# Performance work log

Hardware: AMD Instinct MI355X
Metric: run time of the kernel (lower is better)

Reference implementation:

```python
import jax, jax.numpy as jnp
import numpy as np

B, N, DIM = 4, 1024, 1024
HEADS, DH = 16, 64
INNER = HEADS * DH          # 1024
PROJ_H = max(16, DH // 8)   # 16
TOP_K = 256
TEMP = 1.0
SCALE = DH ** -0.5
LN_EPS = 1e-5


def setup_inputs() -> dict:
    key = jax.random.key(0)
    ks = jax.random.split(key, 9)
    s = 0.02
    return {
        "x": jax.random.normal(ks[0], (B, N, DIM), dtype=jnp.float32),
        "w_qkv": jax.random.normal(ks[1], (3 * INNER, DIM), dtype=jnp.float32) * s,
        "w_out": jax.random.normal(ks[2], (DIM, INNER), dtype=jnp.float32) * s,
        "b_out": jnp.zeros((DIM,), dtype=jnp.float32),
        "ln_g": jnp.ones((DH,), dtype=jnp.float32),
        "ln_b": jnp.zeros((DH,), dtype=jnp.float32),
        "w1": jax.random.normal(ks[3], (PROJ_H, DH), dtype=jnp.float32) * s,
        "b1": jnp.zeros((PROJ_H,), dtype=jnp.float32),
        "w2": jax.random.normal(ks[4], (1, PROJ_H), dtype=jnp.float32) * s,
        "b2": jnp.zeros((1,), dtype=jnp.float32),
    }


def _soma_gate(token_feat, ln_g, ln_b, w1, b1, w2, b2):
    # token_feat: [B, N, DH] -> gate [B, N] in (0,1)
    mu = token_feat.mean(axis=-1, keepdims=True)
    var = token_feat.var(axis=-1, keepdims=True)
    H = (token_feat - mu) * jax.lax.rsqrt(var + LN_EPS) * ln_g + ln_b
    h = jax.nn.gelu(H @ w1.T + b1, approximate=False)
    scores = (h @ w2.T + b2)[..., 0]                       # [B, N]
    scores = scores / (TEMP + 1e-12)
    # top-k soft mask: non-topk positions set to -1e9 before sigmoid
    topk_vals, topk_idx = jax.lax.top_k(scores, TOP_K)
    b_idx = jnp.arange(scores.shape[0])[:, None]
    scores = jnp.full_like(scores, -1e9).at[b_idx, topk_idx].set(topk_vals)
    return jax.nn.sigmoid(scores)


def reference(x, w_qkv, w_out, b_out, ln_g, ln_b, w1, b1, w2, b2):
    Bx, Nx, _ = x.shape
    qkv = x @ w_qkv.T                                      # [B, N, 3*INNER]
    q, k, v = jnp.split(qkv, 3, axis=-1)
    to_heads = lambda t: t.reshape(Bx, Nx, HEADS, DH).transpose(0, 2, 1, 3)
    q, k, v = to_heads(q), to_heads(k), to_heads(v)        # [B, H, N, DH]

    dots = jnp.einsum('bhid,bhjd->bhij', q, k) * SCALE     # [B, H, N, N]

    q_mean = q.mean(axis=1)                                # [B, N, DH]
    gate = _soma_gate(q_mean, ln_g, ln_b, w1, b1, w2, b2)  # [B, N]
    dots = dots * (gate[:, None, :, None] * gate[:, None, None, :])

    attn = jax.nn.softmax(dots, axis=-1)
    out = jnp.einsum('bhij,bhjd->bhid', attn, v)           # [B, H, N, DH]
    out = out.transpose(0, 2, 1, 3).reshape(Bx, Nx, INNER)
    return out @ w_out.T + b_out
```

## Files before the change

kernel.cpp:

```cpp
#include <hip/hip_runtime.h>
#include <hip/hip_bf16.h>
#include <stdint.h>

typedef __bf16 bf16;
typedef __bf16 bf16x8 __attribute__((ext_vector_type(8)));
typedef float floatx4 __attribute__((ext_vector_type(4)));

typedef const __attribute__((address_space(1))) uint32_t glb_u32;
typedef __attribute__((address_space(3))) uint32_t lds_u32;

__device__ __forceinline__ void cp16(void* lds, const void* gp) {
    __builtin_amdgcn_global_load_lds((glb_u32*)gp, (lds_u32*)lds, 16, 0, 0);
}

#define MFMA16(a, b, c) __builtin_amdgcn_mfma_f32_16x16x32_bf16((a), (b), (c), 0, 0, 0)
#define SCALE_ 0.125f

__global__ __launch_bounds__(256) void k_cvt_prep(
    const float* __restrict__ x, const float* __restrict__ wq,
    const float* __restrict__ wo, bf16* __restrict__ xb,
    bf16* __restrict__ xl, bf16* __restrict__ wqb, bf16* __restrict__ wob,
    bf16* __restrict__ whl) {
    if (blockIdx.x < 4096) {
        size_t i8 = ((size_t)blockIdx.x * 256 + threadIdx.x) * 8;
        const float* src; bf16* dst; size_t off; bool isx = false;
        if (i8 < 4194304)      { src = x;  dst = xb;  off = i8; isx = true; }
        else if (i8 < 7340032) { src = wq; dst = wqb; off = i8 - 4194304; }
        else                   { src = wo; dst = wob; off = i8 - 7340032; }
        float4 a = *(const float4*)(src + off);
        float4 b = *(const float4*)(src + off + 4);
        union { bf16 h[8]; uint4 u; } hi, lo;
        hi.h[0] = (bf16)a.x; hi.h[1] = (bf16)a.y; hi.h[2] = (bf16)a.z; hi.h[3] = (bf16)a.w;
        hi.h[4] = (bf16)b.x; hi.h[5] = (bf16)b.y; hi.h[6] = (bf16)b.z; hi.h[7] = (bf16)b.w;
        *(uint4*)(dst + off) = hi.u;
        if (isx) {
            lo.h[0] = (bf16)(a.x - (float)hi.h[0]);
            lo.h[1] = (bf16)(a.y - (float)hi.h[1]);
            lo.h[2] = (bf16)(a.z - (float)hi.h[2]);
            lo.h[3] = (bf16)(a.w - (float)hi.h[3]);
            lo.h[4] = (bf16)(b.x - (float)hi.h[4]);
            lo.h[5] = (bf16)(b.y - (float)hi.h[5]);
            lo.h[6] = (bf16)(b.z - (float)hi.h[6]);
            lo.h[7] = (bf16)(b.w - (float)hi.h[7]);
            *(uint4*)(xl + off) = lo.u;
        }
    } else {
        int t = (blockIdx.x - 4096) * 256 + threadIdx.x;
        int k = t & 1023, d = t >> 10;
        float s = 0.f;
        #pragma unroll
        for (int h = 0; h < 16; ++h) s += wq[(size_t)(h * 64 + d) * 1024 + k];
        s *= (1.f / 16.f);
        bf16 hi = (bf16)s;
        whl[(size_t)d * 1024 + k] = hi;
        whl[(size_t)(64 + d) * 1024 + k] = (bf16)(s - (float)hi);
    }
}

__global__ __launch_bounds__(256) void k_score_gemm(
    const bf16* __restrict__ xh, const bf16* __restrict__ xl,
    const bf16* __restrict__ whl, float* __restrict__ qmbuf) {
    __shared__ bf16 Ah[128 * 32];
    __shared__ bf16 Al[128 * 32];
    __shared__ bf16 Bs[128 * 32];
    const int t = threadIdx.x;
    const int lane = t & 63;
    const int w = t >> 6;
    const int m0 = blockIdx.x * 128;
    const int srow = t >> 2;
    const int scol = (t & 3) * 8;
    const int fr = lane & 15;
    const int kc = (lane >> 4) * 8;
    const int wm0 = w * 32;

    floatx4 zero4 = {0.f, 0.f, 0.f, 0.f};
    floatx4 acc[2][4];
    #pragma unroll
    for (int i = 0; i < 2; ++i)
        #pragma unroll
        for (int j = 0; j < 4; ++j) acc[i][j] = zero4;

    for (int k0 = 0; k0 < 1024; k0 += 32) {
        __syncthreads();
        cp16(Ah + t * 8,        xh + (size_t)(m0 + srow) * 1024 + k0 + scol);
        cp16(Ah + t * 8 + 2048, xh + (size_t)(m0 + srow + 64) * 1024 + k0 + scol);
        cp16(Al + t * 8,        xl + (size_t)(m0 + srow) * 1024 + k0 + scol);
        cp16(Al + t * 8 + 2048, xl + (size_t)(m0 + srow + 64) * 1024 + k0 + scol);
        cp16(Bs + t * 8,        whl + (size_t)srow * 1024 + k0 + scol);
        cp16(Bs + t * 8 + 2048, whl + (size_t)(srow + 64) * 1024 + k0 + scol);
        __syncthreads();
        bf16x8 ah[2], al[2], bh[4], bl[4];
        #pragma unroll
        for (int mi = 0; mi < 2; ++mi) {
            ah[mi] = *(const bf16x8*)&Ah[(wm0 + mi * 16 + fr) * 32 + kc];
            al[mi] = *(const bf16x8*)&Al[(wm0 + mi * 16 + fr) * 32 + kc];
        }
        #pragma unroll
        for (int ni = 0; ni < 4; ++ni) {
            bh[ni] = *(const bf16x8*)&Bs[(ni * 16 + fr) * 32 + kc];
            bl[ni] = *(const bf16x8*)&Bs[(64 + ni * 16 + fr) * 32 + kc];
        }
        #pragma unroll
        for (int mi = 0; mi < 2; ++mi)
            #pragma unroll
            for (int ni = 0; ni < 4; ++ni) {
                acc[mi][ni] = MFMA16(ah[mi], bh[ni], acc[mi][ni]);
                acc[mi][ni] = MFMA16(ah[mi], bl[ni], acc[mi][ni]);
                acc[mi][ni] = MFMA16(al[mi], bh[ni], acc[mi][ni]);
            }
    }

    const int rowb = (lane >> 4) * 4;
    #pragma unroll
    for (int mi = 0; mi < 2; ++mi)
        #pragma unroll
        for (int ni = 0; ni < 4; ++ni)
            #pragma unroll
            for (int r = 0; r < 4; ++r) {
                const int row = m0 + wm0 + mi * 16 + rowb + r;
                qmbuf[(size_t)row * 64 + ni * 16 + fr] = acc[mi][ni][r];
            }
}

__global__ __launch_bounds__(256) void k_score_tail(
    const float* __restrict__ qmbuf, const float* __restrict__ lng,
    const float* __restrict__ lnb, const float* __restrict__ w1f,
    const float* __restrict__ b1f, const float* __restrict__ w2f,
    const float* __restrict__ b2f, float* __restrict__ scores) {
    const int w = threadIdx.x >> 6, lane = threadIdx.x & 63;
    const int r = blockIdx.x * 4 + w;
    __shared__ float Hs[4][64];
    __shared__ float hh[4][16];

    float qm = qmbuf[(size_t)r * 64 + lane];
    float s = qm;
    #pragma unroll
    for (int off = 32; off > 0; off >>= 1) s += __shfl_xor(s, off);
    float mu = s * (1.f / 64.f);
    float dx = qm - mu;
    float v2 = dx * dx;
    #pragma unroll
    for (int off = 32; off > 0; off >>= 1) v2 += __shfl_xor(v2, off);
    float var = v2 * (1.f / 64.f);
    float H = dx * (1.0f / sqrtf(var + 1e-5f)) * lng[lane] + lnb[lane];
    Hs[w][lane] = H;
    if (lane < 16) {
        float a = b1f[lane];
        #pragma unroll
        for (int d = 0; d < 64; ++d) a += Hs[w][d] * w1f[lane * 64 + d];
        hh[w][lane] = 0.5f * a * (1.0f + erff(a * 0.70710678118654752f));
    }
    if (lane == 0) {
        float sc = b2f[0];
        #pragma unroll
        for (int p = 0; p < 16; ++p) sc += hh[w][p] * w2f[p];
        scores[r] = sc;
    }
}

__global__ __launch_bounds__(256) void k_topk(const float* __restrict__ scores,
                                              float* __restrict__ gate,
                                              int* __restrict__ idx,
                                              float* __restrict__ gsel) {
    const int w = threadIdx.x >> 6, lane = threadIdx.x & 63;
    const float* sc = scores + w * 1024;
    float s[16];
    uint32_t key[16];
    #pragma unroll
    for (int i = 0; i < 16; ++i) {
        s[i] = sc[lane * 16 + i];
        uint32_t u = __float_as_uint(s[i]);
        key[i] = (u >> 31) ? ~u : (u | 0x80000000u);
    }
    uint32_t prefix = 0;
    for (int bit = 31; bit >= 0; --bit) {
        uint32_t cand = prefix | (1u << bit);
        int c = 0;
        #pragma unroll
        for (int i = 0; i < 16; ++i) c += (key[i] >= cand);
        #pragma unroll
        for (int off = 1; off < 64; off <<= 1) c += __shfl_xor(c, off);
        if (c >= 256) prefix = cand;
    }
    int cg = 0, eq = 0;
    #pragma unroll
    for (int i = 0; i < 16; ++i) { cg += (key[i] > prefix); eq += (key[i] == prefix); }
    #pragma unroll
    for (int off = 1; off < 64; off <<= 1) cg += __shfl_xor(cg, off);
    const int quota = 256 - cg;
    int xs = eq;
    #pragma unroll
    for (int off = 1; off < 64; off <<= 1) {
        int y = __shfl_up(xs, off);
        if (lane >= off) xs += y;
    }
    int run = xs - eq;
    bool selv[16];
    int cnt = 0;
    #pragma unroll
    for (int i = 0; i < 16; ++i) {
        bool sel = key[i] > prefix;
        if (key[i] == prefix) { sel = (run < quota); run++; }
        selv[i] = sel;
        cnt += sel ? 1 : 0;
        gate[w * 1024 + lane * 16 + i] = sel ? 1.0f / (1.0f + expf(-s[i])) : 0.0f;
    }
    int xc = cnt;
    #pragma unroll
    for (int off = 1; off < 64; off <<= 1) {
        int y = __shfl_up(xc, off);
        if (lane >= off) xc += y;
    }
    int pos = xc - cnt;
    #pragma unroll
    for (int i = 0; i < 16; ++i) {
        if (selv[i]) {
            idx[w * 256 + pos]  = lane * 16 + i;
            gsel[w * 256 + pos] = 1.0f / (1.0f + expf(-s[i]));
            pos++;
        }
    }
}

__global__ __launch_bounds__(256) void k_qkv_sel(
    const bf16* __restrict__ xb, const bf16* __restrict__ wqb,
    const int* __restrict__ idx, bf16* __restrict__ qsel,
    bf16* __restrict__ ksel, bf16* __restrict__ vbuf) {
    __shared__ bf16 As[128 * 32];
    __shared__ bf16 Bs[128 * 32];
    const int t = threadIdx.x;
    const int lane = t & 63;
    const int w = t >> 6;
    const int srow = t >> 2;
    const int scol = (t & 3) * 8;
    const int wm = (w & 1) * 64;
    const int wn = (w >> 1) * 64;
    const int fr = lane & 15;
    const int kc = (lane >> 4) * 8;

    const int bid = blockIdx.x;
    const bool isV = bid < 256;
    int n0, m0;
    size_t abase1, abase2;
    const bf16* Bsrc;
    if (isV) {
        n0 = (bid & 7) * 128;
        m0 = (bid >> 3) * 128;
        Bsrc = wqb + (size_t)(2048 + n0) * 1024;
        abase1 = (size_t)(m0 + srow) * 1024;
        abase2 = (size_t)(m0 + srow + 64) * 1024;
    } else {
        int q = bid - 256;
        n0 = (q & 15) * 128;
        m0 = (q >> 4) * 128;
        Bsrc = wqb + (size_t)n0 * 1024;
        const int mg1 = m0 + srow, mg2 = mg1 + 64;
        const int tok1 = idx[(mg1 >> 8) * 256 + (mg1 & 255)];
        const int tok2 = idx[(mg2 >> 8) * 256 + (mg2 & 255)];
        abase1 = ((size_t)(mg1 >> 8) * 1024 + tok1) * 1024;
        abase2 = ((size_t)(mg2 >> 8) * 1024 + tok2) * 1024;
    }

    floatx4 zero4 = {0.f, 0.f, 0.f, 0.f};
    floatx4 acc[4][4];
    #pragma unroll
    for (int i = 0; i < 4; ++i)
        #pragma unroll
        for (int j = 0; j < 4; ++j) acc[i][j] = zero4;

    for (int k0 = 0; k0 < 1024; k0 += 32) {
        __syncthreads();
        cp16(As + t * 8,        xb + abase1 + k0 + scol);
        cp16(As + t * 8 + 2048, xb + abase2 + k0 + scol);
        cp16(Bs + t * 8,        Bsrc + (size_t)srow * 1024 + k0 + scol);
        cp16(Bs + t * 8 + 2048, Bsrc + (size_t)(srow + 64) * 1024 + k0 + scol);
        __syncthreads();
        bf16x8 a[4], b[4];
        #pragma unroll
        for (int mi = 0; mi < 4; ++mi)
            a[mi] = *(const bf16x8*)&As[(wm + mi * 16 + fr) * 32 + kc];
        #pragma unroll
        for (int ni = 0; ni < 4; ++ni)
            b[ni] = *(const bf16x8*)&Bs[(wn + ni * 16 + fr) * 32 + kc];
        #pragma unroll
        for (int mi = 0; mi < 4; ++mi)
            #pragma unroll
            for (int ni = 0; ni < 4; ++ni)
                acc[mi][ni] = MFMA16(a[mi], b[ni], acc[mi][ni]);
    }

    const int rowb = (lane >> 4) * 4;
    #pragma unroll
    for (int ni = 0; ni < 4; ++ni) {
        const int n_base = n0 + wn + ni * 16;
        if (isV) {
            const int h = n_base >> 6;
            const int dd = (n_base & 63) + fr;
            #pragma unroll
            for (int mi = 0; mi < 4; ++mi)
                #pragma unroll
                for (int r = 0; r < 4; ++r) {
                    const int mg = m0 + wm + mi * 16 + rowb + r;
                    const int bb = mg >> 10, nq = mg & 1023;
                    vbuf[(((size_t)(bb * 16 + h)) * 1024 + nq) * 64 + dd] =
                        (bf16)acc[mi][ni][r];
                }
        } else {
            const int region = n_base >> 10;
            const int nn = n_base & 1023;
            const int h = nn >> 6;
            const int dd = (nn & 63) + fr;
            #pragma unroll
            for (int mi = 0; mi < 4; ++mi)
                #pragma unroll
                for (int r = 0; r < 4; ++r) {
                    const int mg = m0 + wm + mi * 16 + rowb + r;
                    const bf16 v = (bf16)acc[mi][ni][r];
                    if (region == 0) {
                        qsel[(size_t)mg * 1024 + h * 64 + dd] = v;
                    } else {
                        const int b = mg >> 8, s = mg & 255;
                        ksel[(((size_t)(b * 16 + h)) * 256 + s) * 64 + dd] = v;
                    }
                }
        }
    }
}

__global__ __launch_bounds__(256) void k_vgather(
    const bf16* __restrict__ vbuf, const int* __restrict__ idx,
    bf16* __restrict__ VselT, float* __restrict__ SumVuns,
    bf16* __restrict__ qsel) {
    const int bh = blockIdx.x, b = bh >> 4, h = bh & 15;
    const int t = threadIdx.x, w = t >> 6, lane = t & 63;
    const bf16* vb = vbuf + (size_t)bh * 65536;
    bf16* Vo = VselT + (size_t)bh * 16384;

    __shared__ bf16 Vt[64][72];
    __shared__ float redAll[4][64];
    __shared__ float redSel[4][64];

    float sAll = 0.f;
    for (int j = w * 256; j < w * 256 + 256; ++j)
        sAll += (float)vb[(size_t)j * 64 + lane];
    redAll[w][lane] = sAll;

    const int d = t & 63, sg = t >> 6;
    const int s_loc = t >> 2, part = t & 3;
    float sSel = 0.f;

    for (int c = 0; c < 4; ++c) {
        __syncthreads();
        int j = idx[b * 256 + c * 64 + s_loc];
        const uint4* vsrc = (const uint4*)(vb + (size_t)j * 64 + part * 16);
        uint4 v0 = vsrc[0], v1 = vsrc[1];
        *(uint4*)&Vt[s_loc][part * 16]     = v0;
        *(uint4*)&Vt[s_loc][part * 16 + 8] = v1;
        __syncthreads();
        union { bf16 h_[16]; uint4 u[2]; } tmp;
        #pragma unroll
        for (int u = 0; u < 16; ++u) {
            bf16 v = Vt[sg * 16 + u][d];
            tmp.h_[u] = v;
            sSel += (float)v;
        }
        uint4* vdst = (uint4*)(Vo + (size_t)d * 256 + c * 64 + sg * 16);
        vdst[0] = tmp.u[0]; vdst[1] = tmp.u[1];
    }
    redSel[sg][d] = sSel;
    __syncthreads();
    if (t < 64) {
        float sa = redAll[0][t] + redAll[1][t] + redAll[2][t] + redAll[3][t];
        float ss = redSel[0][t] + redSel[1][t] + redSel[2][t] + redSel[3][t];
        SumVuns[bh * 64 + t] = sa - ss;
        qsel[(size_t)(1024 + b) * 1024 + h * 64 + t] = (bf16)(sa * (1.f / 1024.f));
    }
}

__global__ __launch_bounds__(256) void k_attn(
    bf16* __restrict__ qsel, const bf16* __restrict__ Ksel,
    const bf16* __restrict__ VselT, const float* __restrict__ gsel,
    const float* __restrict__ SumVuns) {
    const int bh = blockIdx.x;
    const int qt = blockIdx.y;
    const int b = bh >> 4, h = bh & 15;
    const int t = threadIdx.x, w = t >> 6, lane = t & 63;
    const int m0 = qt * 64;
    const bf16* kb = Ksel + (size_t)bh * 16384;
    const bf16* vb = VselT + (size_t)bh * 16384;

    __shared__ bf16 Qs[64 * 72];
    __shared__ bf16 Ks[64 * 72];
    __shared__ bf16 Vs[64 * 72];
    __shared__ bf16 Ps[4][16 * 72];

    #pragma unroll
    for (int c = 0; c < 2; ++c) {
        int idx2 = t + 256 * c, row = idx2 >> 3, c8 = (idx2 & 7) * 8;
        *(uint4*)&Qs[row * 72 + c8] =
            *(const uint4*)&qsel[(size_t)(b * 256 + m0 + row) * 1024 + h * 64 + c8];
    }
    const int fr = lane & 15;
    const int kq = lane >> 4;
    const int rowb = kq * 4;
    __syncthreads();
    bf16x8 aq[2];
    aq[0] = *(const bf16x8*)&Qs[(w * 16 + fr) * 72 + kq * 8];
    aq[1] = *(const bf16x8*)&Qs[(w * 16 + fr) * 72 + 32 + kq * 8];

    float gq[4];
    #pragma unroll
    for (int r = 0; r < 4; ++r)
        gq[r] = gsel[b * 256 + m0 + w * 16 + rowb + r] * SCALE_;

    float mrow[4] = {0.f, 0.f, 0.f, 0.f};
    float lrow[4] = {0.f, 0.f, 0.f, 0.f};
    floatx4 zero4 = {0.f, 0.f, 0.f, 0.f};
    floatx4 Of[4] = {zero4, zero4, zero4, zero4};

    for (int jt = 0; jt < 4; ++jt) {
        const int j0 = jt * 64;
        __syncthreads();
        #pragma unroll
        for (int c = 0; c < 2; ++c) {
            int idx2 = t + 256 * c, row = idx2 >> 3, c8 = (idx2 & 7) * 8;
            *(uint4*)&Ks[row * 72 + c8] = *(const uint4*)&kb[(size_t)(j0 + row) * 64 + c8];
            *(uint4*)&Vs[row * 72 + c8] = *(const uint4*)&vb[(size_t)row * 256 + j0 + c8];
        }
        __syncthreads();

        floatx4 S[4] = {zero4, zero4, zero4, zero4};
        #pragma unroll
        for (int ks = 0; ks < 2; ++ks) {
            #pragma unroll
            for (int ni = 0; ni < 4; ++ni) {
                bf16x8 bfr = *(const bf16x8*)&Ks[(ni * 16 + fr) * 72 + ks * 32 + kq * 8];
                S[ni] = MFMA16(aq[ks], bfr, S[ni]);
            }
        }
        float gk[4];
        #pragma unroll
        for (int ni = 0; ni < 4; ++ni) gk[ni] = gsel[b * 256 + j0 + ni * 16 + fr];

        float p[4][4], rmax[4] = {0.f, 0.f, 0.f, 0.f};
        #pragma unroll
        for (int ni = 0; ni < 4; ++ni)
            #pragma unroll
            for (int r = 0; r < 4; ++r) {
                float sv = S[ni][r] * (gq[r] * gk[ni]);
                p[ni][r] = sv;
                rmax[r] = fmaxf(rmax[r], sv);
            }
        #pragma unroll
        for (int r = 0; r < 4; ++r) {
            #pragma unroll
            for (int off = 1; off < 16; off <<= 1)
                rmax[r] = fmaxf(rmax[r], __shfl_xor(rmax[r], off));
        }
        float alpha[4], rsum[4] = {0.f, 0.f, 0.f, 0.f};
        #pragma unroll
        for (int r = 0; r < 4; ++r) {
            float mn = fmaxf(mrow[r], rmax[r]);
            alpha[r] = __expf(mrow[r] - mn);
            mrow[r] = mn;
        }
        #pragma unroll
        for (int ni = 0; ni < 4; ++ni)
            #pragma unroll
            for (int r = 0; r < 4; ++r) {
                float pv = __expf(p[ni][r] - mrow[r]);
                p[ni][r] = pv;
                rsum[r] += pv;
            }
        #pragma unroll
        for (int r = 0; r < 4; ++r) {
            #pragma unroll
            for (int off = 1; off < 16; off <<= 1) rsum[r] += __shfl_xor(rsum[r], off);
            lrow[r] = lrow[r] * alpha[r] + rsum[r];
        }
        #pragma unroll
        for (int nd = 0; nd < 4; ++nd)
            #pragma unroll
            for (int r = 0; r < 4; ++r) Of[nd][r] *= alpha[r];

        #pragma unroll
        for (int ni = 0; ni < 4; ++ni)
            #pragma unroll
            for (int r = 0; r < 4; ++r)
                Ps[w][(rowb + r) * 72 + ni * 16 + fr] = (bf16)p[ni][r];

        #pragma unroll
        for (int ks = 0; ks < 2; ++ks) {
            bf16x8 ap = *(const bf16x8*)&Ps[w][fr * 72 + ks * 32 + kq * 8];
            #pragma unroll
            for (int nd = 0; nd < 4; ++nd) {
                bf16x8 bv = *(const bf16x8*)&Vs[(nd * 16 + fr) * 72 + ks * 32 + kq * 8];
                Of[nd] = MFMA16(ap, bv, Of[nd]);
            }
        }
    }

    #pragma unroll
    for (int nd = 0; nd < 4; ++nd)
        #pragma unroll
        for (int r = 0; r < 4; ++r) {
            float em = __expf(-mrow[r]);
            float num = Of[nd][r] + em * SumVuns[bh * 64 + nd * 16 + fr];
            float den = lrow[r] + 768.0f * em;
            qsel[(size_t)(b * 256 + m0 + w * 16 + rowb + r) * 1024 +
                 h * 64 + nd * 16 + fr] = (bf16)(num / den);
        }
}

__global__ __launch_bounds__(256) void k_out_sel(
    const bf16* __restrict__ A, const bf16* __restrict__ wob,
    const float* __restrict__ b_out, const int* __restrict__ idx,
    float* __restrict__ ubase, float* __restrict__ out) {
    __shared__ bf16 As[128 * 32];
    __shared__ bf16 Bs[128 * 32];
    const int t = threadIdx.x;
    const int lane = t & 63;
    const int w = t >> 6;
    const int n0 = blockIdx.x * 128;
    const int m0 = blockIdx.y * 128;
    const bf16* Bsrc = wob + (size_t)n0 * 1024;

    const int srow = t >> 2;
    const int scol = (t & 3) * 8;
    const int wm = (w & 1) * 64;
    const int wn = (w >> 1) * 64;
    const int fr = lane & 15;
    const int kc = (lane >> 4) * 8;

    floatx4 zero4 = {0.f, 0.f, 0.f, 0.f};
    floatx4 acc[4][4];
    #pragma unroll
    for (int i = 0; i < 4; ++i)
        #pragma unroll
        for (int j = 0; j < 4; ++j) acc[i][j] = zero4;

    for (int k0 = 0; k0 < 1024; k0 += 32) {
        __syncthreads();
        cp16(As + t * 8,        A + (size_t)(m0 + srow) * 1024 + k0 + scol);
        cp16(As + t * 8 + 2048, A + (size_t)(m0 + srow + 64) * 1024 + k0 + scol);
        cp16(Bs + t * 8,        Bsrc + (size_t)srow * 1024 + k0 + scol);
        cp16(Bs + t * 8 + 2048, Bsrc + (size_t)(srow + 64) * 1024 + k0 + scol);
        __syncthreads();
        bf16x8 a[4], b[4];
        #pragma unroll
        for (int mi = 0; mi < 4; ++mi)
            a[mi] = *(const bf16x8*)&As[(wm + mi * 16 + fr) * 32 + kc];
        #pragma unroll
        for (int ni = 0; ni < 4; ++ni)
            b[ni] = *(const bf16x8*)&Bs[(wn + ni * 16 + fr) * 32 + kc];
        #pragma unroll
        for (int mi = 0; mi < 4; ++mi)
            #pragma unroll
            for (int ni = 0; ni < 4; ++ni)
                acc[mi][ni] = MFMA16(a[mi], b[ni], acc[mi][ni]);
    }

    const int rowb = (lane >> 4) * 4;
    #pragma unroll
    for (int ni = 0; ni < 4; ++ni) {
        const int ng = n0 + wn + ni * 16 + fr;
        const float bias = b_out[ng];
        #pragma unroll
        for (int mi = 0; mi < 4; ++mi)
            #pragma unroll
            for (int r = 0; r < 4; ++r) {
                const int mg = m0 + wm + mi * 16 + rowb + r;
                const float val = acc[mi][ni][r] + bias;
                if (mg < 1024) {
                    const int b = mg >> 8, s = mg & 255;
                    const int tok = idx[b * 256 + s];
                    out[((size_t)b * 1024 + tok) * 1024 + ng] = val;
                } else if (mg < 1028) {
                    ubase[(size_t)(mg - 1024) * 1024 + ng] = val;
                }
            }
    }
}

__global__ __launch_bounds__(256) void k_fill(
    const float* __restrict__ gate, const float* __restrict__ ubase,
    float* __restrict__ out) {
    const int tokg = blockIdx.x;
    if (gate[tokg] > 0.f) return;
    const int b = tokg >> 10;
    const int c = threadIdx.x * 4;
    *(float4*)(out + (size_t)tokg * 1024 + c) = *(const float4*)(ubase + b * 1024 + c);
}

extern "C" void kernel_launch(void* const* d_in, const int* in_sizes, int n_in,
                              void* d_out, int out_size, void* d_ws, size_t ws_size,
                              hipStream_t stream) {
    const float* x     = (const float*)d_in[0];
    const float* w_qkv = (const float*)d_in[1];
    const float* w_out = (const float*)d_in[2];
    const float* b_out = (const float*)d_in[3];
    const float* ln_g  = (const float*)d_in[4];
    const float* ln_b  = (const float*)d_in[5];
    const float* w1    = (const float*)d_in[6];
    const float* b1    = (const float*)d_in[7];
    const float* w2    = (const float*)d_in[8];
    const float* b2    = (const float*)d_in[9];
    float* out = (float*)d_out;

    char* ws = (char*)d_ws;
    bf16*  qsel  = (bf16*)(ws);
    bf16*  ksel  = (bf16*)(ws + 4194304);
    bf16*  VselT = (bf16*)(ws + 6291456);
    bf16*  vbuf  = (bf16*)(ws + 8388608);
    bf16*  xb    = (bf16*)(ws + 16777216);
    bf16*  wqb   = (bf16*)(ws + 25165824);
    bf16*  wob   = (bf16*)(ws + 31457280);
    int*   idx     = (int*)(ws + 33554432);
    float* gsel    = (float*)(ws + 33558528);
    float* scores  = (float*)(ws + 33562624);
    float* gate    = (float*)(ws + 33579008);
    float* SumVuns = (float*)(ws + 33595392);
    float* ubase   = (float*)(ws + 33611776);
    bf16*  whl     = (bf16*)(ws + 33685504);
    float* qmbuf   = (float*)(ws + 34603008);
    bf16*  xlbuf   = (bf16*)(ws + 35651584);

    k_cvt_prep<<<4352, 256, 0, stream>>>(x, w_qkv, w_out, xb, xlbuf, wqb, wob, whl);
    k_score_gemm<<<32, 256, 0, stream>>>(xb, xlbuf, whl, qmbuf);
    k_score_tail<<<1024, 256, 0, stream>>>(qmbuf, ln_g, ln_b, w1, b1, w2, b2, scores);
    k_topk<<<1, 256, 0, stream>>>(scores, gate, idx, gsel);
    k_qkv_sel<<<384, 256, 0, stream>>>(xb, wqb, idx, qsel, ksel, vbuf);
    k_vgather<<<64, 256, 0, stream>>>(vbuf, idx, VselT, SumVuns, qsel);
    k_attn<<<dim3(64, 4), 256, 0, stream>>>(qsel, ksel, VselT, gsel, SumVuns);
    k_out_sel<<<dim3(8, 9), 256, 0, stream>>>(qsel, wob, b_out, idx, ubase, out);
    k_fill<<<4096, 256, 0, stream>>>(gate, ubase, out);
}
```

Measured before the change: 228.7 us.

## Compute V only for selected tokens and get sum of V via linearity

Full V projection for all 4096 tokens is replaced by computing V only for the 256 selected tokens per batch. The total V sum is obtained by first summing x over tokens (new reduction kernels), then multiplying that summed row, split into bf16 hi/lo parts, through the V weights as extra rows in the same GEMM. This cuts the V GEMM work by roughly 4x and removes the full vbuf write and reread in the gather kernel. The cost is two small extra kernels that read x in fp32, plus a padded extra M tile (9 row tiles, only 8 rows useful) in the selection GEMM.

Measured after the change: 229.9 us. Within noise of the previous version (+0.5%).

```diff
diff --git a/kernel.cpp b/kernel.cpp
--- a/kernel.cpp
+++ b/kernel.cpp
@@ -57,6 +57,32 @@
     }
 }
 
+__global__ __launch_bounds__(256) void k_xsum(const float* __restrict__ x,
+                                              float* __restrict__ partial) {
+    const int g = blockIdx.x;
+    const int b = g >> 4, rg = g & 15;
+    const size_t base = ((size_t)b * 1024 + rg * 64) * 1024;
+    const int c = threadIdx.x * 4;
+    float4 acc = {0.f, 0.f, 0.f, 0.f};
+    for (int i = 0; i < 64; ++i) {
+        float4 xv = *(const float4*)(x + base + (size_t)i * 1024 + c);
+        acc.x += xv.x; acc.y += xv.y; acc.z += xv.z; acc.w += xv.w;
+    }
+    *(float4*)(partial + (size_t)g * 1024 + c) = acc;
+}
+
+__global__ __launch_bounds__(256) void k_xsum2(const float* __restrict__ partial,
+                                               bf16* __restrict__ xsumhl) {
+    const int o = blockIdx.x * 256 + threadIdx.x;
+    const int b = o >> 10, k = o & 1023;
+    float s = 0.f;
+    #pragma unroll
+    for (int g = 0; g < 16; ++g) s += partial[(size_t)(b * 16 + g) * 1024 + k];
+    bf16 hi = (bf16)s;
+    xsumhl[(size_t)b * 1024 + k] = hi;
+    xsumhl[(size_t)(4 + b) * 1024 + k] = (bf16)(s - (float)hi);
+}
+
 __global__ __launch_bounds__(256) void k_score_gemm(
     const bf16* __restrict__ xh, const bf16* __restrict__ xl,
     const bf16* __restrict__ whl, float* __restrict__ qmbuf) {
@@ -224,13 +250,18 @@
 
 __global__ __launch_bounds__(256) void k_qkv_sel(
     const bf16* __restrict__ xb, const bf16* __restrict__ wqb,
-    const int* __restrict__ idx, bf16* __restrict__ qsel,
-    bf16* __restrict__ ksel, bf16* __restrict__ vbuf) {
+    const int* __restrict__ idx, const bf16* __restrict__ xsumhl,
+    bf16* __restrict__ qsel, bf16* __restrict__ ksel,
+    bf16* __restrict__ vsel, float* __restrict__ SumVparts) {
     __shared__ bf16 As[128 * 32];
     __shared__ bf16 Bs[128 * 32];
     const int t = threadIdx.x;
     const int lane = t & 63;
     const int w = t >> 6;
+    const int n0 = blockIdx.x * 128;
+    const int m0 = blockIdx.y * 128;
+    const bf16* Bsrc = wqb + (size_t)n0 * 1024;
+
     const int srow = t >> 2;
     const int scol = (t & 3) * 8;
     const int wm = (w & 1) * 64;
@@ -238,28 +269,17 @@
     const int fr = lane & 15;
     const int kc = (lane >> 4) * 8;
 
-    const int bid = blockIdx.x;
-    const bool isV = bid < 256;
-    int n0, m0;
-    size_t abase1, abase2;
-    const bf16* Bsrc;
-    if (isV) {
-        n0 = (bid & 7) * 128;
-        m0 = (bid >> 3) * 128;
-        Bsrc = wqb + (size_t)(2048 + n0) * 1024;
-        abase1 = (size_t)(m0 + srow) * 1024;
-        abase2 = (size_t)(m0 + srow + 64) * 1024;
-    } else {
-        int q = bid - 256;
-        n0 = (q & 15) * 128;
-        m0 = (q >> 4) * 128;
-        Bsrc = wqb + (size_t)n0 * 1024;
-        const int mg1 = m0 + srow, mg2 = mg1 + 64;
-        const int tok1 = idx[(mg1 >> 8) * 256 + (mg1 & 255)];
-        const int tok2 = idx[(mg2 >> 8) * 256 + (mg2 & 255)];
-        abase1 = ((size_t)(mg1 >> 8) * 1024 + tok1) * 1024;
-        abase2 = ((size_t)(mg2 >> 8) * 1024 + tok2) * 1024;
-    }
+    const int mg1 = m0 + srow, mg2 = mg1 + 64;
+    const bf16* ap1;
+    const bf16* ap2;
+    if (mg1 < 1024)
+        ap1 = xb + ((size_t)(mg1 >> 8) * 1024 + idx[(mg1 >> 8) * 256 + (mg1 & 255)]) * 1024;
+    else if (mg1 < 1032) ap1 = xsumhl + (size_t)(mg1 - 1024) * 1024;
+    else ap1 = xb;
+    if (mg2 < 1024)
+        ap2 = xb + ((size_t)(mg2 >> 8) * 1024 + idx[(mg2 >> 8) * 256 + (mg2 & 255)]) * 1024;
+    else if (mg2 < 1032) ap2 = xsumhl + (size_t)(mg2 - 1024) * 1024;
+    else ap2 = xb;
 
     floatx4 zero4 = {0.f, 0.f, 0.f, 0.f};
     floatx4 acc[4][4];
@@ -270,8 +290,8 @@
 
     for (int k0 = 0; k0 < 1024; k0 += 32) {
         __syncthreads();
-        cp16(As + t * 8,        xb + abase1 + k0 + scol);
-        cp16(As + t * 8 + 2048, xb + abase2 + k0 + scol);
+        cp16(As + t * 8,        ap1 + k0 + scol);
+        cp16(As + t * 8 + 2048, ap2 + k0 + scol);
         cp16(Bs + t * 8,        Bsrc + (size_t)srow * 1024 + k0 + scol);
         cp16(Bs + t * 8 + 2048, Bsrc + (size_t)(srow + 64) * 1024 + k0 + scol);
         __syncthreads();
@@ -293,57 +313,44 @@
     #pragma unroll
     for (int ni = 0; ni < 4; ++ni) {
         const int n_base = n0 + wn + ni * 16;
-        if (isV) {
-            const int h = n_base >> 6;
-            const int dd = (n_base & 63) + fr;
-            #pragma unroll
-            for (int mi = 0; mi < 4; ++mi)
-                #pragma unroll
-                for (int r = 0; r < 4; ++r) {
-                    const int mg = m0 + wm + mi * 16 + rowb + r;
-                    const int bb = mg >> 10, nq = mg & 1023;
-                    vbuf[(((size_t)(bb * 16 + h)) * 1024 + nq) * 64 + dd] =
-                        (bf16)acc[mi][ni][r];
+        const int region = n_base >> 10;
+        const int nn = n_base & 1023;
+        const int h = nn >> 6;
+        const int dd = (nn & 63) + fr;
+        #pragma unroll
+        for (int mi = 0; mi < 4; ++mi) {
+            #pragma unroll
+            for (int r = 0; r < 4; ++r) {
+                const int mg = m0 + wm + mi * 16 + rowb + r;
+                const float av = acc[mi][ni][r];
+                if (mg < 1024) {
+                    const int b = mg >> 8, s = mg & 255;
+                    const bf16 v = (bf16)av;
+                    if (region == 0)
+                        qsel[(size_t)mg * 1024 + h * 64 + dd] = v;
+                    else if (region == 1)
+                        ksel[(((size_t)(b * 16 + h)) * 256 + s) * 64 + dd] = v;
+                    else
+                        vsel[(((size_t)(b * 16 + h)) * 256 + s) * 64 + dd] = v;
+                } else if (mg < 1032 && region == 2) {
+                    SumVparts[(size_t)(mg - 1024) * 1024 + h * 64 + dd] = av;
                 }
-        } else {
-            const int region = n_base >> 10;
-            const int nn = n_base & 1023;
-            const int h = nn >> 6;
-            const int dd = (nn & 63) + fr;
-            #pragma unroll
-            for (int mi = 0; mi < 4; ++mi)
-                #pragma unroll
-                for (int r = 0; r < 4; ++r) {
-                    const int mg = m0 + wm + mi * 16 + rowb + r;
-                    const bf16 v = (bf16)acc[mi][ni][r];
-                    if (region == 0) {
-                        qsel[(size_t)mg * 1024 + h * 64 + dd] = v;
-                    } else {
-                        const int b = mg >> 8, s = mg & 255;
-                        ksel[(((size_t)(b * 16 + h)) * 256 + s) * 64 + dd] = v;
-                    }
-                }
+            }
         }
     }
 }
 
 __global__ __launch_bounds__(256) void k_vgather(
-    const bf16* __restrict__ vbuf, const int* __restrict__ idx,
+    const bf16* __restrict__ vsel, const float* __restrict__ SumVparts,
     bf16* __restrict__ VselT, float* __restrict__ SumVuns,
     bf16* __restrict__ qsel) {
     const int bh = blockIdx.x, b = bh >> 4, h = bh & 15;
-    const int t = threadIdx.x, w = t >> 6, lane = t & 63;
-    const bf16* vb = vbuf + (size_t)bh * 65536;
+    const int t = threadIdx.x;
+    const bf16* vb = vsel + (size_t)bh * 16384;
     bf16* Vo = VselT + (size_t)bh * 16384;
 
     __shared__ bf16 Vt[64][72];
-    __shared__ float redAll[4][64];
     __shared__ float redSel[4][64];
-
-    float sAll = 0.f;
-    for (int j = w * 256; j < w * 256 + 256; ++j)
-        sAll += (float)vb[(size_t)j * 64 + lane];
-    redAll[w][lane] = sAll;
 
     const int d = t & 63, sg = t >> 6;
     const int s_loc = t >> 2, part = t & 3;
@@ -351,8 +358,7 @@
 
     for (int c = 0; c < 4; ++c) {
         __syncthreads();
-        int j = idx[b * 256 + c * 64 + s_loc];
-        const uint4* vsrc = (const uint4*)(vb + (size_t)j * 64 + part * 16);
+        const uint4* vsrc = (const uint4*)(vb + (size_t)(c * 64 + s_loc) * 64 + part * 16);
         uint4 v0 = vsrc[0], v1 = vsrc[1];
         *(uint4*)&Vt[s_loc][part * 16]     = v0;
         *(uint4*)&Vt[s_loc][part * 16 + 8] = v1;
@@ -370,7 +376,8 @@
     redSel[sg][d] = sSel;
     __syncthreads();
     if (t < 64) {
-        float sa = redAll[0][t] + redAll[1][t] + redAll[2][t] + redAll[3][t];
+        float sa = SumVparts[(size_t)b * 1024 + h * 64 + t] +
+                   SumVparts[(size_t)(4 + b) * 1024 + h * 64 + t];
         float ss = redSel[0][t] + redSel[1][t] + redSel[2][t] + redSel[3][t];
         SumVuns[bh * 64 + t] = sa - ss;
         qsel[(size_t)(1024 + b) * 1024 + h * 64 + t] = (bf16)(sa * (1.f / 1024.f));
@@ -611,7 +618,10 @@
     bf16*  qsel  = (bf16*)(ws);
     bf16*  ksel  = (bf16*)(ws + 4194304);
     bf16*  VselT = (bf16*)(ws + 6291456);
-    bf16*  vbuf  = (bf16*)(ws + 8388608);
+    bf16*  vsel  = (bf16*)(ws + 8388608);
+    float* partial   = (float*)(ws + 10485760);
+    float* SumVparts = (float*)(ws + 10747904);
+    bf16*  xsumhl    = (bf16*)(ws + 10780672);
     bf16*  xb    = (bf16*)(ws + 16777216);
     bf16*  wqb   = (bf16*)(ws + 25165824);
     bf16*  wob   = (bf16*)(ws + 31457280);
@@ -626,11 +636,14 @@
     bf16*  xlbuf   = (bf16*)(ws + 35651584);
 
     k_cvt_prep<<<4352, 256, 0, stream>>>(x, w_qkv, w_out, xb, xlbuf, wqb, wob, whl);
+    k_xsum<<<64, 256, 0, stream>>>(x, partial);
+    k_xsum2<<<16, 256, 0, stream>>>(partial, xsumhl);
     k_score_gemm<<<32, 256, 0, stream>>>(xb, xlbuf, whl, qmbuf);
     k_score_tail<<<1024, 256, 0, stream>>>(qmbuf, ln_g, ln_b, w1, b1, w2, b2, scores);
     k_topk<<<1, 256, 0, stream>>>(scores, gate, idx, gsel);
-    k_qkv_sel<<<384, 256, 0, stream>>>(xb, wqb, idx, qsel, ksel, vbuf);
-    k_vgather<<<64, 256, 0, stream>>>(vbuf, idx, VselT, SumVuns, qsel);
+    k_qkv_sel<<<dim3(24, 9), 256, 0, stream>>>(xb, wqb, idx, xsumhl, qsel, ksel,
+                                               vsel, SumVparts);
+    k_vgather<<<64, 256, 0, stream>>>(vsel, SumVparts, VselT, SumVuns, qsel);
     k_attn<<<dim3(64, 4), 256, 0, stream>>>(qsel, ksel, VselT, gsel, SumVuns);
     k_out_sel<<<dim3(8, 9), 256, 0, stream>>>(qsel, wob, b_out, idx, ubase, out);
     k_fill<<<4096, 256, 0, stream>>>(gate, ubase, out);
```
